# Kernel tuning notes

Measured on AMD Instinct MI355X. Metric: run time of the kernel, lower is better.

## Reference

```python
import jax, jax.numpy as jnp
import numpy as np

H = 64
EPS = 1e-5


def _lstm_layer(x, w_ih, w_hh, b_ih, b_hh):
    """Single LSTM layer, batch_first input x: [B, T, I]. PyTorch gate order i,f,g,o."""
    B, T, _ = x.shape
    # precompute input contributions for all timesteps: [B, T, 4H]
    xw = jnp.einsum('bti,gi->btg', x, w_ih) + (b_ih + b_hh)
    xw = jnp.swapaxes(xw, 0, 1)  # [T, B, 4H] for scan over time

    def step(carry, xw_t):
        h, c = carry
        gates = xw_t + h @ w_hh.T  # [B, 4H]
        i, f, g, o = jnp.split(gates, 4, axis=-1)
        i = jax.nn.sigmoid(i)
        f = jax.nn.sigmoid(f)
        g = jnp.tanh(g)
        o = jax.nn.sigmoid(o)
        c = f * c + i * g
        h = o * jnp.tanh(c)
        return (h, c), h

    h0 = jnp.zeros((B, H), x.dtype)
    (_, _), hs = jax.lax.scan(step, (h0, h0), xw)
    return jnp.swapaxes(hs, 0, 1)  # [B, T, H]


def setup_inputs() -> dict:
    key = jax.random.key(0)
    ks = jax.random.split(key, 16)
    B, T, F = 4096, 256, 32
    s = 1.0 / np.sqrt(H)  # PyTorch LSTM init scale
    inp = {
        'x': jax.random.normal(ks[0], (B, T, F), jnp.float32),
        'w_ih0': jax.random.uniform(ks[1], (4 * H, F), jnp.float32, -s, s),
        'w_hh0': jax.random.uniform(ks[2], (4 * H, H), jnp.float32, -s, s),
        'b_ih0': jax.random.uniform(ks[3], (4 * H,), jnp.float32, -s, s),
        'b_hh0': jax.random.uniform(ks[4], (4 * H,), jnp.float32, -s, s),
        'w_ih1': jax.random.uniform(ks[5], (4 * H, H), jnp.float32, -s, s),
        'w_hh1': jax.random.uniform(ks[6], (4 * H, H), jnp.float32, -s, s),
        'b_ih1': jax.random.uniform(ks[7], (4 * H,), jnp.float32, -s, s),
        'b_hh1': jax.random.uniform(ks[8], (4 * H,), jnp.float32, -s, s),
        'ln_g': jnp.ones((H,), jnp.float32),
        'ln_b': jnp.zeros((H,), jnp.float32),
        'w1': jax.random.uniform(ks[9], (64, H), jnp.float32, -s, s),
        'b1': jax.random.uniform(ks[10], (64,), jnp.float32, -s, s),
        'w2': jax.random.uniform(ks[11], (1, 64), jnp.float32, -0.125, 0.125),
        'b2': jax.random.uniform(ks[12], (1,), jnp.float32, -0.125, 0.125),
    }
    return inp


def reference(x, w_ih0, w_hh0, b_ih0, b_hh0, w_ih1, w_hh1, b_ih1, b_hh1,
              ln_g, ln_b, w1, b1, w2, b2):
    out0 = _lstm_layer(x, w_ih0, w_hh0, b_ih0, b_hh0)      # [B, T, H]
    out1 = _lstm_layer(out0, w_ih1, w_hh1, b_ih1, b_hh1)   # [B, T, H]
    last = out1[:, -1, :]                                   # [B, H]
    # LayerNorm
    mu = jnp.mean(last, axis=-1, keepdims=True)
    var = jnp.mean(jnp.square(last - mu), axis=-1, keepdims=True)
    ln = (last - mu) * jax.lax.rsqrt(var + EPS) * ln_g + ln_b
    # MLP head
    h = jax.nn.relu(ln @ w1.T + b1)
    y = h @ w2.T + b2                                       # [B, 1]
    return y[:, 0]
```

## Files before the change

kernel.cpp:

```cpp
#include <hip/hip_runtime.h>

#define TSEQ 256
#define FIN  32
#define HID  64

typedef _Float16 f16x8 __attribute__((ext_vector_type(8)));
typedef float    f32x4 __attribute__((ext_vector_type(4)));

__device__ __forceinline__ float sigm(float x) {
    return __builtin_amdgcn_rcpf(1.0f + __expf(-x));
}
__device__ __forceinline__ float tanh_fast(float x) {
    float e = __expf(2.0f * x);
    return 1.0f - 2.0f * __builtin_amdgcn_rcpf(e + 1.0f);
}
__device__ __forceinline__ float wsum(float v) {
    #pragma unroll
    for (int off = 32; off > 0; off >>= 1) v += __shfl_xor(v, off, 64);
    return v;
}

__global__ __launch_bounds__(1024, 4)
void lstm_fused(const float* __restrict__ x,
                const float* __restrict__ w_ih0, const float* __restrict__ w_hh0,
                const float* __restrict__ b_ih0, const float* __restrict__ b_hh0,
                const float* __restrict__ w_ih1, const float* __restrict__ w_hh1,
                const float* __restrict__ b_ih1, const float* __restrict__ b_hh1,
                const float* __restrict__ ln_g, const float* __restrict__ ln_b,
                const float* __restrict__ w1, const float* __restrict__ b1,
                const float* __restrict__ w2, const float* __restrict__ b2,
                float* __restrict__ out)
{
    __shared__ __align__(16) _Float16 X[2][16][32];
    __shared__ __align__(16) _Float16 H0[2][16][72];
    __shared__ __align__(16) _Float16 H1[2][16][72];
    __shared__ __align__(16) float HF[16][68];
    __shared__ __align__(16) float LNB[16][64];

    const int tid  = threadIdx.x;
    const int wave = tid >> 6;
    const int lane = tid & 63;
    const int q    = lane >> 4;
    const int lm   = lane & 15;
    const int q8   = q * 8;
    const int b0   = blockIdx.x * 16;

    const int np  = wave * 16 + lm;
    const int drow = np >> 2;
    const int ty   = np & 3;
    const int row  = ty * 64 + drow;
    const int dq   = wave * 4 + q;

    f16x8 w0f[3], w1f[4];
    f32x4 bias0, bias1;
    {
        const float* p0 = w_ih0 + row * FIN + q8;
        const float* p1 = w_hh0 + row * HID + q8;
        const float* p2 = w_hh0 + row * HID + 32 + q8;
        const float* p3 = w_ih1 + row * HID + q8;
        const float* p4 = w_ih1 + row * HID + 32 + q8;
        const float* p5 = w_hh1 + row * HID + q8;
        const float* p6 = w_hh1 + row * HID + 32 + q8;
        #pragma unroll
        for (int j = 0; j < 8; ++j) {
            w0f[0][j] = (_Float16)p0[j];
            w0f[1][j] = (_Float16)p1[j];
            w0f[2][j] = (_Float16)p2[j];
            w1f[0][j] = (_Float16)p3[j];
            w1f[1][j] = (_Float16)p4[j];
            w1f[2][j] = (_Float16)p5[j];
            w1f[3][j] = (_Float16)p6[j];
        }
        #pragma unroll
        for (int r = 0; r < 4; ++r) {
            bias0[r] = b_ih0[r * 64 + dq] + b_hh0[r * 64 + dq];
            bias1[r] = b_ih1[r * 64 + dq] + b_hh1[r * 64 + dq];
        }
    }

    for (int i = tid; i < 2 * 16 * 72; i += 1024) {
        ((_Float16*)H0)[i] = (_Float16)0.0f;
        ((_Float16*)H1)[i] = (_Float16)0.0f;
    }
    const bool xthr = tid < 512;
    const int xrow = (tid >> 5) & 15, xcol = tid & 31;
    const float* xbase = x + (size_t)(b0 + xrow) * TSEQ * FIN + xcol;
    float xw = 0.0f;
    if (xthr) {
        X[0][xrow][xcol] = (_Float16)xbase[0];
        xw = xbase[FIN];
    }
    float c0 = 0.0f, c1 = 0.0f;
    __syncthreads();

    for (int t = 0; t < TSEQ; ++t) {
        const int pt = t & 1;

        float xnew = 0.0f;
        if (xthr && t + 2 < TSEQ) xnew = xbase[(size_t)(t + 2) * FIN];

        {
            f16x8 bx  = *reinterpret_cast<const f16x8*>(&X[pt][lm][q8]);
            f16x8 bha = *reinterpret_cast<const f16x8*>(&H0[pt ^ 1][lm][q8]);
            f16x8 bhb = *reinterpret_cast<const f16x8*>(&H0[pt ^ 1][lm][32 + q8]);
            f32x4 a = bias0;
            a = __builtin_amdgcn_mfma_f32_16x16x32_f16(w0f[0], bx,  a, 0, 0, 0);
            a = __builtin_amdgcn_mfma_f32_16x16x32_f16(w0f[1], bha, a, 0, 0, 0);
            a = __builtin_amdgcn_mfma_f32_16x16x32_f16(w0f[2], bhb, a, 0, 0, 0);
            float ig = sigm(a[0]);
            float fg = sigm(a[1]);
            float gg = tanh_fast(a[2]);
            float og = sigm(a[3]);
            c0 = fg * c0 + ig * gg;
            float h = og * tanh_fast(c0);
            H0[pt][lm][dq] = (_Float16)h;
        }
        if (xthr && t + 1 < TSEQ) X[pt ^ 1][xrow][xcol] = (_Float16)xw;
        xw = xnew;
        __syncthreads();

        {
            f16x8 b0a = *reinterpret_cast<const f16x8*>(&H0[pt][lm][q8]);
            f16x8 b0b = *reinterpret_cast<const f16x8*>(&H0[pt][lm][32 + q8]);
            f16x8 b1a = *reinterpret_cast<const f16x8*>(&H1[pt ^ 1][lm][q8]);
            f16x8 b1b = *reinterpret_cast<const f16x8*>(&H1[pt ^ 1][lm][32 + q8]);
            f32x4 a = bias1;
            a = __builtin_amdgcn_mfma_f32_16x16x32_f16(w1f[0], b0a, a, 0, 0, 0);
            a = __builtin_amdgcn_mfma_f32_16x16x32_f16(w1f[1], b0b, a, 0, 0, 0);
            a = __builtin_amdgcn_mfma_f32_16x16x32_f16(w1f[2], b1a, a, 0, 0, 0);
            a = __builtin_amdgcn_mfma_f32_16x16x32_f16(w1f[3], b1b, a, 0, 0, 0);
            float ig = sigm(a[0]);
            float fg = sigm(a[1]);
            float gg = tanh_fast(a[2]);
            float og = sigm(a[3]);
            c1 = fg * c1 + ig * gg;
            float h = og * tanh_fast(c1);
            H1[pt][lm][dq] = (_Float16)h;
            if (t == TSEQ - 1) HF[lm][dq] = h;
        }
        __syncthreads();
    }

    const float lngv = ln_g[lane], lnbv = ln_b[lane];
    const float b1v = b1[lane], w2v = w2[lane];
    const float* w1row = w1 + lane * 64;
    {
        float v  = HF[wave][lane];
        float mu = wsum(v) * (1.0f / 64.0f);
        float dv = v - mu;
        float var = wsum(dv * dv) * (1.0f / 64.0f);
        float ln = dv * rsqrtf(var + 1e-5f) * lngv + lnbv;
        LNB[wave][lane] = ln;
        float s = b1v;
        #pragma unroll
        for (int dd = 0; dd < 64; ++dd)
            s = fmaf(LNB[wave][dd], w1row[dd], s);
        s = fmaxf(s, 0.0f);
        float y = wsum(s * w2v);
        if (lane == 0) out[b0 + wave] = y + b2[0];
    }
}

extern "C" void kernel_launch(void* const* d_in, const int* in_sizes, int n_in,
                              void* d_out, int out_size, void* d_ws, size_t ws_size,
                              hipStream_t stream) {
    const float* x     = (const float*)d_in[0];
    const float* w_ih0 = (const float*)d_in[1];
    const float* w_hh0 = (const float*)d_in[2];
    const float* b_ih0 = (const float*)d_in[3];
    const float* b_hh0 = (const float*)d_in[4];
    const float* w_ih1 = (const float*)d_in[5];
    const float* w_hh1 = (const float*)d_in[6];
    const float* b_ih1 = (const float*)d_in[7];
    const float* b_hh1 = (const float*)d_in[8];
    const float* ln_g  = (const float*)d_in[9];
    const float* ln_b  = (const float*)d_in[10];
    const float* w1    = (const float*)d_in[11];
    const float* b1    = (const float*)d_in[12];
    const float* w2    = (const float*)d_in[13];
    const float* b2    = (const float*)d_in[14];
    lstm_fused<<<dim3(256), dim3(1024), 0, stream>>>(
        x, w_ih0, w_hh0, b_ih0, b_hh0,
        w_ih1, w_hh1, b_ih1, b_hh1,
        ln_g, ln_b, w1, b1, w2, b2, (float*)d_out);
}
```

Baseline: 428.1 us.

## Skew layer-1 LSTM one step behind layer 0 to halve barriers

Restructures the time loop so that in iteration i, layer 0 computes step i while layer 1 computes step i-1, both reading shared state written in the previous iteration. This removes one of the two __syncthreads per timestep and lets the MFMA chains and activations of both layers interleave. The cost is one extra loop iteration with predicated work and slightly higher register pressure from holding both accumulators.

```diff
diff --git a/kernel.cpp b/kernel.cpp
--- a/kernel.cpp
+++ b/kernel.cpp
@@ -45,7 +45,7 @@
     const int q8   = q * 8;
     const int b0   = blockIdx.x * 16;
 
-    const int np  = wave * 16 + lm;
+    const int np   = wave * 16 + lm;
     const int drow = np >> 2;
     const int ty   = np & 3;
     const int row  = ty * 64 + drow;
@@ -93,51 +93,54 @@
     float c0 = 0.0f, c1 = 0.0f;
     __syncthreads();
 
-    for (int t = 0; t < TSEQ; ++t) {
-        const int pt = t & 1;
+    for (int i = 0; i <= TSEQ; ++i) {
+        const int p = i & 1;
 
         float xnew = 0.0f;
-        if (xthr && t + 2 < TSEQ) xnew = xbase[(size_t)(t + 2) * FIN];
+        if (xthr && i + 2 < TSEQ) xnew = xbase[(size_t)(i + 2) * FIN];
 
-        {
-            f16x8 bx  = *reinterpret_cast<const f16x8*>(&X[pt][lm][q8]);
-            f16x8 bha = *reinterpret_cast<const f16x8*>(&H0[pt ^ 1][lm][q8]);
-            f16x8 bhb = *reinterpret_cast<const f16x8*>(&H0[pt ^ 1][lm][32 + q8]);
-            f32x4 a = bias0;
-            a = __builtin_amdgcn_mfma_f32_16x16x32_f16(w0f[0], bx,  a, 0, 0, 0);
-            a = __builtin_amdgcn_mfma_f32_16x16x32_f16(w0f[1], bha, a, 0, 0, 0);
-            a = __builtin_amdgcn_mfma_f32_16x16x32_f16(w0f[2], bhb, a, 0, 0, 0);
-            float ig = sigm(a[0]);
-            float fg = sigm(a[1]);
-            float gg = tanh_fast(a[2]);
-            float og = sigm(a[3]);
+        f16x8 rx   = *reinterpret_cast<const f16x8*>(&X[p][lm][q8]);
+        f16x8 rh0a = *reinterpret_cast<const f16x8*>(&H0[p ^ 1][lm][q8]);
+        f16x8 rh0b = *reinterpret_cast<const f16x8*>(&H0[p ^ 1][lm][32 + q8]);
+        f16x8 rh1a = *reinterpret_cast<const f16x8*>(&H1[p][lm][q8]);
+        f16x8 rh1b = *reinterpret_cast<const f16x8*>(&H1[p][lm][32 + q8]);
+
+        f32x4 aA, aB;
+        if (i < TSEQ) {
+            aA = bias0;
+            aA = __builtin_amdgcn_mfma_f32_16x16x32_f16(w0f[0], rx,   aA, 0, 0, 0);
+            aA = __builtin_amdgcn_mfma_f32_16x16x32_f16(w0f[1], rh0a, aA, 0, 0, 0);
+            aA = __builtin_amdgcn_mfma_f32_16x16x32_f16(w0f[2], rh0b, aA, 0, 0, 0);
+        }
+        if (i >= 1) {
+            aB = bias1;
+            aB = __builtin_amdgcn_mfma_f32_16x16x32_f16(w1f[0], rh0a, aB, 0, 0, 0);
+            aB = __builtin_amdgcn_mfma_f32_16x16x32_f16(w1f[1], rh0b, aB, 0, 0, 0);
+            aB = __builtin_amdgcn_mfma_f32_16x16x32_f16(w1f[2], rh1a, aB, 0, 0, 0);
+            aB = __builtin_amdgcn_mfma_f32_16x16x32_f16(w1f[3], rh1b, aB, 0, 0, 0);
+        }
+
+        if (i < TSEQ) {
+            float ig = sigm(aA[0]);
+            float fg = sigm(aA[1]);
+            float gg = tanh_fast(aA[2]);
+            float og = sigm(aA[3]);
             c0 = fg * c0 + ig * gg;
             float h = og * tanh_fast(c0);
-            H0[pt][lm][dq] = (_Float16)h;
+            H0[p][lm][dq] = (_Float16)h;
         }
-        if (xthr && t + 1 < TSEQ) X[pt ^ 1][xrow][xcol] = (_Float16)xw;
-        xw = xnew;
-        __syncthreads();
-
-        {
-            f16x8 b0a = *reinterpret_cast<const f16x8*>(&H0[pt][lm][q8]);
-            f16x8 b0b = *reinterpret_cast<const f16x8*>(&H0[pt][lm][32 + q8]);
-            f16x8 b1a = *reinterpret_cast<const f16x8*>(&H1[pt ^ 1][lm][q8]);
-            f16x8 b1b = *reinterpret_cast<const f16x8*>(&H1[pt ^ 1][lm][32 + q8]);
-            f32x4 a = bias1;
-            a = __builtin_amdgcn_mfma_f32_16x16x32_f16(w1f[0], b0a, a, 0, 0, 0);
-            a = __builtin_amdgcn_mfma_f32_16x16x32_f16(w1f[1], b0b, a, 0, 0, 0);
-            a = __builtin_amdgcn_mfma_f32_16x16x32_f16(w1f[2], b1a, a, 0, 0, 0);
-            a = __builtin_amdgcn_mfma_f32_16x16x32_f16(w1f[3], b1b, a, 0, 0, 0);
-            float ig = sigm(a[0]);
-            float fg = sigm(a[1]);
-            float gg = tanh_fast(a[2]);
-            float og = sigm(a[3]);
+        if (i >= 1) {
+            float ig = sigm(aB[0]);
+            float fg = sigm(aB[1]);
+            float gg = tanh_fast(aB[2]);
+            float og = sigm(aB[3]);
             c1 = fg * c1 + ig * gg;
             float h = og * tanh_fast(c1);
-            H1[pt][lm][dq] = (_Float16)h;
-            if (t == TSEQ - 1) HF[lm][dq] = h;
+            H1[p ^ 1][lm][dq] = (_Float16)h;
+            if (i == TSEQ) HF[lm][dq] = h;
         }
+        if (xthr && i + 1 < TSEQ) X[p ^ 1][xrow][xcol] = (_Float16)xw;
+        xw = xnew;
         __syncthreads();
     }
 
```

Measured after the change: 389.1 us. -9.1%, faster.
